# Kernel tuning notes

Measured on AMD Instinct MI355X. Metric: run time of the kernel, lower is better.

Reference implementation:

```python
import jax, jax.numpy as jnp
import numpy as np

B, D, H, E, C, TOPK = 16384, 2048, 2048, 6, 1024, 3

def setup_inputs() -> dict:
    key = jax.random.key(0)
    ks = jax.random.split(key, 8)
    s_d = 1.0 / np.sqrt(D)
    s_h = 1.0 / np.sqrt(H)
    return {
        "x": jax.random.normal(ks[0], (B, D), dtype=jnp.float32),
        "gate_W": jax.random.uniform(ks[1], (E, D), jnp.float32, -s_d, s_d),
        "gate_b": jax.random.uniform(ks[2], (E,), jnp.float32, -s_d, s_d),
        "W1": jax.random.uniform(ks[3], (E, H, D), jnp.float32, -s_d, s_d),
        "b1": jax.random.uniform(ks[4], (E, H), jnp.float32, -s_d, s_d),
        "W2": jax.random.uniform(ks[5], (E, C, H), jnp.float32, -s_h, s_h),
        "b2": jax.random.uniform(ks[6], (E, C), jnp.float32, -s_h, s_h),
    }

def reference(x, gate_W, gate_b, W1, b1, W2, b2):
    # gating: top-k sparse softmax
    gate_logits = x @ gate_W.T + gate_b                      # [B, E]
    topk_vals, topk_idx = jax.lax.top_k(gate_logits, TOPK)   # [B, K]
    neg_inf = jnp.finfo(gate_logits.dtype).min
    sparse = jnp.full_like(gate_logits, neg_inf)
    rows = jnp.arange(gate_logits.shape[0])[:, None]
    sparse = sparse.at[rows, topk_idx].set(topk_vals)
    gw = jax.nn.softmax(sparse, axis=-1)                     # [B, E]
    # dense experts: Linear -> GELU (exact, erf) -> Linear (dropout is eval no-op)
    h = jnp.einsum('bd,ehd->beh', x, W1) + b1[None]          # [B, E, H]
    h = jax.nn.gelu(h, approximate=False)
    expert_outs = jnp.einsum('beh,ech->bec', h, W2) + b2[None]  # [B, E, C]
    out = jnp.einsum('be,bec->bc', gw, expert_outs)          # masked combine
    return (out, gw)
```

## Files before the change

### kernel.cpp

```cpp
#include <hip/hip_runtime.h>
#include <hip/hip_bf16.h>
#include <math.h>

#define B_ 16384
#define D_ 2048
#define H_ 2048
#define E_ 6
#define C_ 1024

typedef __attribute__((ext_vector_type(8))) short short8;
typedef __attribute__((ext_vector_type(4))) float f32x4;

__device__ __forceinline__ unsigned short f2bf(float f) {
    __hip_bfloat16 h = __float2bfloat16(f);
    return *reinterpret_cast<unsigned short*>(&h);
}

__device__ __forceinline__ void async_copy16(const unsigned short* g, unsigned short* l) {
    __builtin_amdgcn_global_load_lds(
        (const __attribute__((address_space(1))) unsigned int*)(g),
        (__attribute__((address_space(3))) unsigned int*)(l), 16, 0, 0);
}

__global__ void gate_kernel(const float* __restrict__ x, const float* __restrict__ gW,
                            const float* __restrict__ gb, float* __restrict__ gw_out,
                            int* __restrict__ counts, int* __restrict__ rowlist,
                            float* __restrict__ wtslist) {
    int wave = threadIdx.x >> 6;
    int lane = threadIdx.x & 63;
    int row  = blockIdx.x * 4 + wave;
    const float* xr = x + (size_t)row * D_;
    double acc[E_] = {0, 0, 0, 0, 0, 0};
    for (int i = 0; i < D_ / 64; ++i) {
        int d = i * 64 + lane;
        double xv = (double)xr[d];
#pragma unroll
        for (int e = 0; e < E_; ++e) acc[e] += xv * (double)gW[e * D_ + d];
    }
#pragma unroll
    for (int off = 32; off > 0; off >>= 1) {
#pragma unroll
        for (int e = 0; e < E_; ++e) acc[e] += __shfl_down(acc[e], off);
    }
    if (lane == 0) {
        double lg[E_];
#pragma unroll
        for (int e = 0; e < E_; ++e) lg[e] = acc[e] + (double)gb[e];
        bool used[E_] = {false, false, false, false, false, false};
        int idx[3]; double val[3];
        for (int k = 0; k < 3; ++k) {
            int best = -1; double bv = -1e300;
            for (int e = 0; e < E_; ++e)
                if (!used[e] && lg[e] > bv) { bv = lg[e]; best = e; }
            used[best] = true; idx[k] = best; val[k] = bv;
        }
        double m = val[0];
        double w[3]; double s = 0.0;
        for (int k = 0; k < 3; ++k) { w[k] = exp(val[k] - m); s += w[k]; }
        float gwv[E_] = {0.f, 0.f, 0.f, 0.f, 0.f, 0.f};
        for (int k = 0; k < 3; ++k) gwv[idx[k]] = (float)(w[k] / s);
#pragma unroll
        for (int e = 0; e < E_; ++e) gw_out[(size_t)row * E_ + e] = gwv[e];
        for (int k = 0; k < 3; ++k) {
            int e = idx[k];
            int pos = atomicAdd(&counts[e], 1);
            rowlist[(size_t)e * B_ + pos] = row * 3 + k;
            wtslist[(size_t)e * B_ + pos] = (float)(w[k] / s);
        }
    }
}

__global__ void cast_f32_bf16(const float* __restrict__ in, unsigned short* __restrict__ out, int n4) {
    int i = blockIdx.x * blockDim.x + threadIdx.x;
    if (i < n4) {
        float4 v = ((const float4*)in)[i];
        ushort4 u;
        u.x = f2bf(v.x); u.y = f2bf(v.y); u.z = f2bf(v.z); u.w = f2bf(v.w);
        ((ushort4*)out)[i] = u;
    }
}

__global__ __launch_bounds__(256) void gemm1_kernel(
    const unsigned short* __restrict__ xb, const unsigned short* __restrict__ W1b,
    const float* __restrict__ b1, const int* __restrict__ counts,
    const int* __restrict__ rowlist, unsigned short* __restrict__ hbuf) {
    int e = blockIdx.z;
    int cnt = counts[e];
    int m0 = blockIdx.y * 128;
    if (m0 >= cnt) return;
    int n0 = blockIdx.x * 128;

    __shared__ __align__(16) unsigned short At[128 * 64];
    __shared__ __align__(16) unsigned short Bt[128 * 64];
    int tid = threadIdx.x;
    const int* rlist = rowlist + (size_t)e * B_;

    const unsigned short* aptr[4];
    const unsigned short* bptr[4];
#pragma unroll
    for (int it = 0; it < 4; ++it) {
        int seg = it * 256 + tid;
        int r = seg >> 3, c = seg & 7;
        int cs = c ^ (r & 7);
        int idx = m0 + r; if (idx >= cnt) idx = cnt - 1;
        aptr[it] = xb + (size_t)(rlist[idx] / 3) * D_ + cs * 8;
        bptr[it] = W1b + (size_t)e * H_ * D_ + (size_t)(n0 + r) * D_ + cs * 8;
    }
    int lane = tid & 63;
    int wv = tid >> 6;
    int wm = (wv & 1) * 64;
    int wn = (wv >> 1) * 64;
    int fm = lane & 15;
    int kg = lane >> 4;
    int fsw = fm & 7;
    f32x4 acc[4][4] = {};

    for (int k0 = 0; k0 < D_; k0 += 64) {
#pragma unroll
        for (int it = 0; it < 4; ++it) {
            async_copy16(aptr[it] + k0, At + (it * 256 + tid) * 8);
            async_copy16(bptr[it] + k0, Bt + (it * 256 + tid) * 8);
        }
        __syncthreads();
#pragma unroll
        for (int kk = 0; kk < 2; ++kk) {
            int g = kk * 4 + kg;
            int go = (g ^ fsw) * 8;
            short8 af[4], bfr[4];
#pragma unroll
            for (int mi = 0; mi < 4; ++mi)
                af[mi] = *(const short8*)(At + (wm + mi * 16 + fm) * 64 + go);
#pragma unroll
            for (int ni = 0; ni < 4; ++ni)
                bfr[ni] = *(const short8*)(Bt + (wn + ni * 16 + fm) * 64 + go);
#pragma unroll
            for (int mi = 0; mi < 4; ++mi)
#pragma unroll
                for (int ni = 0; ni < 4; ++ni)
                    acc[mi][ni] = __builtin_amdgcn_mfma_f32_16x16x32_bf16(af[mi], bfr[ni], acc[mi][ni], 0, 0, 0);
        }
        __syncthreads();
    }

    int rlim = cnt - m0;
#pragma unroll
    for (int mi = 0; mi < 4; ++mi) {
#pragma unroll
        for (int i = 0; i < 4; ++i) {
            int r = wm + mi * 16 + kg * 4 + i;
            if (r < rlim) {
                size_t base = (size_t)rlist[m0 + r] * H_ + n0;
#pragma unroll
                for (int ni = 0; ni < 4; ++ni) {
                    int col = wn + ni * 16 + fm;
                    float v = acc[mi][ni][i] + b1[e * H_ + n0 + col];
                    v = 0.5f * v * (1.0f + erff(v * 0.70710678118654752f));
                    hbuf[base + col] = f2bf(v);
                }
            }
        }
    }
}

__global__ __launch_bounds__(256) void gemm2_kernel(
    const unsigned short* __restrict__ hbuf, const unsigned short* __restrict__ W2b,
    const float* __restrict__ b2, const int* __restrict__ counts,
    const int* __restrict__ rowlist, const float* __restrict__ wtslist,
    float* __restrict__ out) {
    int e = blockIdx.z;
    int cnt = counts[e];
    int m0 = blockIdx.y * 128;
    if (m0 >= cnt) return;
    int n0 = blockIdx.x * 128;

    __shared__ __align__(16) unsigned short At[128 * 64];
    __shared__ __align__(16) unsigned short Bt[128 * 64];
    int tid = threadIdx.x;
    const int* rlist = rowlist + (size_t)e * B_;
    const float* wlist = wtslist + (size_t)e * B_;

    const unsigned short* aptr[4];
    const unsigned short* bptr[4];
#pragma unroll
    for (int it = 0; it < 4; ++it) {
        int seg = it * 256 + tid;
        int r = seg >> 3, c = seg & 7;
        int cs = c ^ (r & 7);
        int idx = m0 + r; if (idx >= cnt) idx = cnt - 1;
        aptr[it] = hbuf + (size_t)rlist[idx] * H_ + cs * 8;
        bptr[it] = W2b + (size_t)e * C_ * H_ + (size_t)(n0 + r) * H_ + cs * 8;
    }
    int lane = tid & 63;
    int wv = tid >> 6;
    int wm = (wv & 1) * 64;
    int wn = (wv >> 1) * 64;
    int fm = lane & 15;
    int kg = lane >> 4;
    int fsw = fm & 7;
    f32x4 acc[4][4] = {};

    for (int k0 = 0; k0 < H_; k0 += 64) {
#pragma unroll
        for (int it = 0; it < 4; ++it) {
            async_copy16(aptr[it] + k0, At + (it * 256 + tid) * 8);
            async_copy16(bptr[it] + k0, Bt + (it * 256 + tid) * 8);
        }
        __syncthreads();
#pragma unroll
        for (int kk = 0; kk < 2; ++kk) {
            int g = kk * 4 + kg;
            int go = (g ^ fsw) * 8;
            short8 af[4], bfr[4];
#pragma unroll
            for (int mi = 0; mi < 4; ++mi)
                af[mi] = *(const short8*)(At + (wm + mi * 16 + fm) * 64 + go);
#pragma unroll
            for (int ni = 0; ni < 4; ++ni)
                bfr[ni] = *(const short8*)(Bt + (wn + ni * 16 + fm) * 64 + go);
#pragma unroll
            for (int mi = 0; mi < 4; ++mi)
#pragma unroll
                for (int ni = 0; ni < 4; ++ni)
                    acc[mi][ni] = __builtin_amdgcn_mfma_f32_16x16x32_bf16(af[mi], bfr[ni], acc[mi][ni], 0, 0, 0);
        }
        __syncthreads();
    }

    int rlim = cnt - m0;
#pragma unroll
    for (int mi = 0; mi < 4; ++mi) {
#pragma unroll
        for (int i = 0; i < 4; ++i) {
            int r = wm + mi * 16 + kg * 4 + i;
            if (r < rlim) {
                float w = wlist[m0 + r];
                float* orow = out + (size_t)(rlist[m0 + r] / 3) * C_ + n0;
#pragma unroll
                for (int ni = 0; ni < 4; ++ni) {
                    int col = wn + ni * 16 + fm;
                    float v = (acc[mi][ni][i] + b2[e * C_ + n0 + col]) * w;
                    atomicAdd(&orow[col], v);
                }
            }
        }
    }
}

extern "C" void kernel_launch(void* const* d_in, const int* in_sizes, int n_in,
                              void* d_out, int out_size, void* d_ws, size_t ws_size,
                              hipStream_t stream) {
    const float* x  = (const float*)d_in[0];
    const float* gW = (const float*)d_in[1];
    const float* gb = (const float*)d_in[2];
    const float* W1 = (const float*)d_in[3];
    const float* b1 = (const float*)d_in[4];
    const float* W2 = (const float*)d_in[5];
    const float* b2 = (const float*)d_in[6];
    float* out    = (float*)d_out;
    float* gw_out = out + (size_t)B_ * C_;

    char* ws = (char*)d_ws;
    size_t off = 0;
    auto alloc = [&](size_t bytes) -> char* {
        char* p = ws + off;
        off = (off + bytes + 255) & ~(size_t)255;
        return p;
    };
    int*            counts  = (int*)alloc(E_ * 4);
    int*            rowlist = (int*)alloc((size_t)E_ * B_ * 4);
    float*          wtslist = (float*)alloc((size_t)E_ * B_ * 4);
    unsigned short* xb      = (unsigned short*)alloc((size_t)B_ * D_ * 2);
    unsigned short* W1b     = (unsigned short*)alloc((size_t)E_ * H_ * D_ * 2);
    unsigned short* W2b     = (unsigned short*)alloc((size_t)E_ * C_ * H_ * 2);
    unsigned short* hbuf    = (unsigned short*)alloc((size_t)3 * B_ * H_ * 2);
    (void)ws_size; (void)in_sizes; (void)n_in; (void)out_size;

    hipMemsetAsync(counts, 0, E_ * 4, stream);
    hipMemsetAsync(out, 0, (size_t)B_ * C_ * 4, stream);

    gate_kernel<<<B_ / 4, 256, 0, stream>>>(x, gW, gb, gw_out, counts, rowlist, wtslist);
    cast_f32_bf16<<<(B_ * D_ / 4) / 256, 256, 0, stream>>>(x, xb, B_ * D_ / 4);
    cast_f32_bf16<<<(E_ * H_ * D_ / 4) / 256, 256, 0, stream>>>(W1, W1b, E_ * H_ * D_ / 4);
    cast_f32_bf16<<<(E_ * C_ * H_ / 4) / 256, 256, 0, stream>>>(W2, W2b, E_ * C_ * H_ / 4);
    gemm1_kernel<<<dim3(H_ / 128, B_ / 128, E_), 256, 0, stream>>>(xb, W1b, b1, counts, rowlist, hbuf);
    gemm2_kernel<<<dim3(C_ / 128, B_ / 128, E_), 256, 0, stream>>>(hbuf, W2b, b2, counts, rowlist, wtslist, out);
}
```

Measured before the change: 2.089 ms.

## Triple-buffer GEMM pipeline with 256x128 tiles and replace atomics with slot combine

Rewrites both expert GEMM kernels to use 512-thread blocks over 256x128 tiles with a three-stage LDS ring buffer. Async global-to-LDS loads for step t+2 are interleaved with the MFMA work of step t, using explicit waitcnt, barriers and setprio. GEMM2 writes weighted per-slot results to a scratch buffer when workspace permits, and a separate combine kernel sums the three slots instead of using atomicAdd on the output. The aim is to hide memory latency, increase operand reuse and remove atomic contention. In exchange it uses more LDS (limiting occupancy), adds a large scratch write/read pass, and its correctness depends on hand-tuned wait counts.

```diff
diff --git a/kernel.cpp b/kernel.cpp
--- a/kernel.cpp
+++ b/kernel.cpp
@@ -80,79 +80,144 @@
     }
 }
 
-__global__ __launch_bounds__(256) void gemm1_kernel(
+
+#define GEMM_PROLOGUE_AND_LOOP(KDIM)                                                     \
+    int lane = tid & 63;                                                                 \
+    int wv   = tid >> 6;                                                                 \
+    int wrow = (wv >> 1) * 64;                                                           \
+    int wcol = (wv & 1) * 64;                                                            \
+    int fm   = lane & 15;                                                                \
+    int kg   = lane >> 4;                                                                \
+    int fsw  = fm & 7;                                                                   \
+    f32x4 acc[4][4] = {};                                                                \
+    unsigned short* A0 = As;                unsigned short* Bq0 = Bs;                    \
+    unsigned short* A1 = As + 256 * 64;     unsigned short* Bq1 = Bs + 128 * 64;         \
+    unsigned short* A2 = As + 2 * 256 * 64; unsigned short* Bq2 = Bs + 2 * 128 * 64;     \
+    _Pragma("unroll")                                                                    \
+    for (int it = 0; it < 4; ++it) async_copy16(aptr[it], A0 + (it * 512 + tid) * 8);    \
+    _Pragma("unroll")                                                                    \
+    for (int it = 0; it < 2; ++it) async_copy16(bptr[it], Bq0 + (it * 512 + tid) * 8);   \
+    _Pragma("unroll")                                                                    \
+    for (int it = 0; it < 4; ++it) async_copy16(aptr[it] + 64, A1 + (it * 512 + tid) * 8); \
+    _Pragma("unroll")                                                                    \
+    for (int it = 0; it < 2; ++it) async_copy16(bptr[it] + 64, Bq1 + (it * 512 + tid) * 8); \
+    asm volatile("s_waitcnt vmcnt(6)" ::: "memory");                                     \
+    __builtin_amdgcn_s_barrier();                                                        \
+    __builtin_amdgcn_sched_barrier(0);                                                   \
+    const int NT = (KDIM) / 64;                                                          \
+    for (int t = 0; t < NT; ++t) {                                                       \
+        const bool st  = (t + 2 < NT);                                                   \
+        const int  k0s = (t + 2) * 64;                                                   \
+        {                                              \
+            short8 aF[4], bF[4];                                                         \
+            int go = (kg ^ fsw) * 8;                                                     \
+            _Pragma("unroll")                                                            \
+            for (int mi = 0; mi < 4; ++mi)                                               \
+                aF[mi] = *(const short8*)(A0 + (wrow + mi * 16 + fm) * 64 + go);         \
+            _Pragma("unroll")                                                            \
+            for (int ni = 0; ni < 4; ++ni)                                               \
+                bF[ni] = *(const short8*)(Bq0 + (wcol + ni * 16 + fm) * 64 + go);        \
+            if (st) {                                                                    \
+                async_copy16(aptr[0] + k0s, A2 + (0 * 512 + tid) * 8);                   \
+                async_copy16(aptr[1] + k0s, A2 + (1 * 512 + tid) * 8);                   \
+                async_copy16(bptr[0] + k0s, Bq2 + (0 * 512 + tid) * 8);                  \
+            }                                                                            \
+            __builtin_amdgcn_s_barrier();                                                \
+            asm volatile("s_waitcnt lgkmcnt(0)" ::: "memory");                           \
+            __builtin_amdgcn_sched_barrier(0);                                           \
+            __builtin_amdgcn_s_setprio(1);                                               \
+            _Pragma("unroll")                                                            \
+            for (int mi = 0; mi < 4; ++mi)                                               \
+                _Pragma("unroll")                                                        \
+                for (int ni = 0; ni < 4; ++ni)                                           \
+                    acc[mi][ni] = __builtin_amdgcn_mfma_f32_16x16x32_bf16(               \
+                        aF[mi], bF[ni], acc[mi][ni], 0, 0, 0);                           \
+            __builtin_amdgcn_s_setprio(0);                                               \
+            __builtin_amdgcn_s_barrier();                                                \
+            __builtin_amdgcn_sched_barrier(0);                                           \
+        }                                                                                \
+        {                                              \
+            short8 aF[4], bF[4];                                                         \
+            int go = ((4 + kg) ^ fsw) * 8;                                               \
+            _Pragma("unroll")                                                            \
+            for (int mi = 0; mi < 4; ++mi)                                               \
+                aF[mi] = *(const short8*)(A0 + (wrow + mi * 16 + fm) * 64 + go);         \
+            _Pragma("unroll")                                                            \
+            for (int ni = 0; ni < 4; ++ni)                                               \
+                bF[ni] = *(const short8*)(Bq0 + (wcol + ni * 16 + fm) * 64 + go);        \
+            if (st) {                                                                    \
+                async_copy16(aptr[2] + k0s, A2 + (2 * 512 + tid) * 8);                   \
+                async_copy16(aptr[3] + k0s, A2 + (3 * 512 + tid) * 8);                   \
+                async_copy16(bptr[1] + k0s, Bq2 + (1 * 512 + tid) * 8);                  \
+            }                                                                            \
+            __builtin_amdgcn_s_barrier();                                                \
+            asm volatile("s_waitcnt lgkmcnt(0)" ::: "memory");                           \
+            __builtin_amdgcn_sched_barrier(0);                                           \
+            __builtin_amdgcn_s_setprio(1);                                               \
+            _Pragma("unroll")                                                            \
+            for (int mi = 0; mi < 4; ++mi)                                               \
+                _Pragma("unroll")                                                        \
+                for (int ni = 0; ni < 4; ++ni)                                           \
+                    acc[mi][ni] = __builtin_amdgcn_mfma_f32_16x16x32_bf16(               \
+                        aF[mi], bF[ni], acc[mi][ni], 0, 0, 0);                           \
+            __builtin_amdgcn_s_setprio(0);                                               \
+        }                                                                                \
+           \
+        if (st) asm volatile("s_waitcnt vmcnt(6)" ::: "memory");                         \
+        else    asm volatile("s_waitcnt vmcnt(0)" ::: "memory");                         \
+        __builtin_amdgcn_s_barrier();                                                    \
+        __builtin_amdgcn_sched_barrier(0);                                               \
+        unsigned short* tA = A0; A0 = A1; A1 = A2; A2 = tA;                              \
+        unsigned short* tB = Bq0; Bq0 = Bq1; Bq1 = Bq2; Bq2 = tB;                        \
+    }
+
+__global__ __launch_bounds__(512, 2) void gemm1_kernel(
     const unsigned short* __restrict__ xb, const unsigned short* __restrict__ W1b,
     const float* __restrict__ b1, const int* __restrict__ counts,
     const int* __restrict__ rowlist, unsigned short* __restrict__ hbuf) {
     int e = blockIdx.z;
     int cnt = counts[e];
-    int m0 = blockIdx.y * 128;
+    int m0 = blockIdx.y * 256;
     if (m0 >= cnt) return;
     int n0 = blockIdx.x * 128;
 
-    __shared__ __align__(16) unsigned short At[128 * 64];
-    __shared__ __align__(16) unsigned short Bt[128 * 64];
+    __shared__ __align__(16) unsigned short As[3 * 256 * 64];
+    __shared__ __align__(16) unsigned short Bs[3 * 128 * 64];
+
     int tid = threadIdx.x;
     const int* rlist = rowlist + (size_t)e * B_;
 
     const unsigned short* aptr[4];
-    const unsigned short* bptr[4];
+    const unsigned short* bptr[2];
 #pragma unroll
     for (int it = 0; it < 4; ++it) {
-        int seg = it * 256 + tid;
+        int seg = it * 512 + tid;
         int r = seg >> 3, c = seg & 7;
         int cs = c ^ (r & 7);
         int idx = m0 + r; if (idx >= cnt) idx = cnt - 1;
         aptr[it] = xb + (size_t)(rlist[idx] / 3) * D_ + cs * 8;
+    }
+#pragma unroll
+    for (int it = 0; it < 2; ++it) {
+        int seg = it * 512 + tid;
+        int r = seg >> 3, c = seg & 7;
+        int cs = c ^ (r & 7);
         bptr[it] = W1b + (size_t)e * H_ * D_ + (size_t)(n0 + r) * D_ + cs * 8;
     }
-    int lane = tid & 63;
-    int wv = tid >> 6;
-    int wm = (wv & 1) * 64;
-    int wn = (wv >> 1) * 64;
-    int fm = lane & 15;
-    int kg = lane >> 4;
-    int fsw = fm & 7;
-    f32x4 acc[4][4] = {};
-
-    for (int k0 = 0; k0 < D_; k0 += 64) {
-#pragma unroll
-        for (int it = 0; it < 4; ++it) {
-            async_copy16(aptr[it] + k0, At + (it * 256 + tid) * 8);
-            async_copy16(bptr[it] + k0, Bt + (it * 256 + tid) * 8);
-        }
-        __syncthreads();
-#pragma unroll
-        for (int kk = 0; kk < 2; ++kk) {
-            int g = kk * 4 + kg;
-            int go = (g ^ fsw) * 8;
-            short8 af[4], bfr[4];
-#pragma unroll
-            for (int mi = 0; mi < 4; ++mi)
-                af[mi] = *(const short8*)(At + (wm + mi * 16 + fm) * 64 + go);
-#pragma unroll
-            for (int ni = 0; ni < 4; ++ni)
-                bfr[ni] = *(const short8*)(Bt + (wn + ni * 16 + fm) * 64 + go);
-#pragma unroll
-            for (int mi = 0; mi < 4; ++mi)
-#pragma unroll
-                for (int ni = 0; ni < 4; ++ni)
-                    acc[mi][ni] = __builtin_amdgcn_mfma_f32_16x16x32_bf16(af[mi], bfr[ni], acc[mi][ni], 0, 0, 0);
-        }
-        __syncthreads();
-    }
+
+    GEMM_PROLOGUE_AND_LOOP(D_)
 
     int rlim = cnt - m0;
 #pragma unroll
     for (int mi = 0; mi < 4; ++mi) {
 #pragma unroll
         for (int i = 0; i < 4; ++i) {
-            int r = wm + mi * 16 + kg * 4 + i;
+            int r = wrow + mi * 16 + kg * 4 + i;
             if (r < rlim) {
                 size_t base = (size_t)rlist[m0 + r] * H_ + n0;
 #pragma unroll
                 for (int ni = 0; ni < 4; ++ni) {
-                    int col = wn + ni * 16 + fm;
+                    int col = wcol + ni * 16 + fm;
                     float v = acc[mi][ni][i] + b1[e * H_ + n0 + col];
                     v = 0.5f * v * (1.0f + erff(v * 0.70710678118654752f));
                     hbuf[base + col] = f2bf(v);
@@ -162,88 +227,84 @@
     }
 }
 
-__global__ __launch_bounds__(256) void gemm2_kernel(
+__global__ __launch_bounds__(512, 2) void gemm2_kernel(
     const unsigned short* __restrict__ hbuf, const unsigned short* __restrict__ W2b,
     const float* __restrict__ b2, const int* __restrict__ counts,
     const int* __restrict__ rowlist, const float* __restrict__ wtslist,
-    float* __restrict__ out) {
+    float* __restrict__ sbuf, float* __restrict__ out) {
     int e = blockIdx.z;
     int cnt = counts[e];
-    int m0 = blockIdx.y * 128;
+    int m0 = blockIdx.y * 256;
     if (m0 >= cnt) return;
     int n0 = blockIdx.x * 128;
 
-    __shared__ __align__(16) unsigned short At[128 * 64];
-    __shared__ __align__(16) unsigned short Bt[128 * 64];
+    __shared__ __align__(16) unsigned short As[3 * 256 * 64];
+    __shared__ __align__(16) unsigned short Bs[3 * 128 * 64];
+
     int tid = threadIdx.x;
     const int* rlist = rowlist + (size_t)e * B_;
     const float* wlist = wtslist + (size_t)e * B_;
 
     const unsigned short* aptr[4];
-    const unsigned short* bptr[4];
+    const unsigned short* bptr[2];
 #pragma unroll
     for (int it = 0; it < 4; ++it) {
-        int seg = it * 256 + tid;
+        int seg = it * 512 + tid;
         int r = seg >> 3, c = seg & 7;
         int cs = c ^ (r & 7);
         int idx = m0 + r; if (idx >= cnt) idx = cnt - 1;
         aptr[it] = hbuf + (size_t)rlist[idx] * H_ + cs * 8;
+    }
+#pragma unroll
+    for (int it = 0; it < 2; ++it) {
+        int seg = it * 512 + tid;
+        int r = seg >> 3, c = seg & 7;
+        int cs = c ^ (r & 7);
         bptr[it] = W2b + (size_t)e * C_ * H_ + (size_t)(n0 + r) * H_ + cs * 8;
     }
-    int lane = tid & 63;
-    int wv = tid >> 6;
-    int wm = (wv & 1) * 64;
-    int wn = (wv >> 1) * 64;
-    int fm = lane & 15;
-    int kg = lane >> 4;
-    int fsw = fm & 7;
-    f32x4 acc[4][4] = {};
-
-    for (int k0 = 0; k0 < H_; k0 += 64) {
-#pragma unroll
-        for (int it = 0; it < 4; ++it) {
-            async_copy16(aptr[it] + k0, At + (it * 256 + tid) * 8);
-            async_copy16(bptr[it] + k0, Bt + (it * 256 + tid) * 8);
-        }
-        __syncthreads();
-#pragma unroll
-        for (int kk = 0; kk < 2; ++kk) {
-            int g = kk * 4 + kg;
-            int go = (g ^ fsw) * 8;
-            short8 af[4], bfr[4];
-#pragma unroll
-            for (int mi = 0; mi < 4; ++mi)
-                af[mi] = *(const short8*)(At + (wm + mi * 16 + fm) * 64 + go);
-#pragma unroll
-            for (int ni = 0; ni < 4; ++ni)
-                bfr[ni] = *(const short8*)(Bt + (wn + ni * 16 + fm) * 64 + go);
-#pragma unroll
-            for (int mi = 0; mi < 4; ++mi)
-#pragma unroll
-                for (int ni = 0; ni < 4; ++ni)
-                    acc[mi][ni] = __builtin_amdgcn_mfma_f32_16x16x32_bf16(af[mi], bfr[ni], acc[mi][ni], 0, 0, 0);
-        }
-        __syncthreads();
-    }
+
+    GEMM_PROLOGUE_AND_LOOP(H_)
 
     int rlim = cnt - m0;
 #pragma unroll
     for (int mi = 0; mi < 4; ++mi) {
 #pragma unroll
         for (int i = 0; i < 4; ++i) {
-            int r = wm + mi * 16 + kg * 4 + i;
+            int r = wrow + mi * 16 + kg * 4 + i;
             if (r < rlim) {
-                float w = wlist[m0 + r];
-                float* orow = out + (size_t)(rlist[m0 + r] / 3) * C_ + n0;
-#pragma unroll
-                for (int ni = 0; ni < 4; ++ni) {
-                    int col = wn + ni * 16 + fm;
-                    float v = (acc[mi][ni][i] + b2[e * C_ + n0 + col]) * w;
-                    atomicAdd(&orow[col], v);
+                int slot = rlist[m0 + r];
+                float w  = wlist[m0 + r];
+                if (sbuf) {
+                    float* srow = sbuf + (size_t)slot * C_ + n0;
+#pragma unroll
+                    for (int ni = 0; ni < 4; ++ni) {
+                        int col = wcol + ni * 16 + fm;
+                        srow[col] = (acc[mi][ni][i] + b2[e * C_ + n0 + col]) * w;
+                    }
+                } else {
+                    float* orow = out + (size_t)(slot / 3) * C_ + n0;
+#pragma unroll
+                    for (int ni = 0; ni < 4; ++ni) {
+                        int col = wcol + ni * 16 + fm;
+                        atomicAdd(&orow[col], (acc[mi][ni][i] + b2[e * C_ + n0 + col]) * w);
+                    }
                 }
             }
         }
     }
+}
+
+__global__ void combine_kernel(const float* __restrict__ sbuf, float* __restrict__ out) {
+    int i   = blockIdx.x * 256 + threadIdx.x;
+    int row = i >> 8;
+    int c4  = i & 255;
+    const float4* s4 = (const float4*)sbuf;
+    size_t b = (size_t)row * 3 * 256 + c4;
+    float4 a = s4[b], d = s4[b + 256], g = s4[b + 512];
+    float4 r;
+    r.x = a.x + d.x + g.x; r.y = a.y + d.y + g.y;
+    r.z = a.z + d.z + g.z; r.w = a.w + d.w + g.w;
+    ((float4*)out)[i] = r;
 }
 
 extern "C" void kernel_launch(void* const* d_in, const int* in_sizes, int n_in,
@@ -273,15 +334,20 @@
     unsigned short* W1b     = (unsigned short*)alloc((size_t)E_ * H_ * D_ * 2);
     unsigned short* W2b     = (unsigned short*)alloc((size_t)E_ * C_ * H_ * 2);
     unsigned short* hbuf    = (unsigned short*)alloc((size_t)3 * B_ * H_ * 2);
-    (void)ws_size; (void)in_sizes; (void)n_in; (void)out_size;
+    float*          sbuf    = (float*)alloc((size_t)3 * B_ * C_ * 4);
+    bool use_sbuf = (ws_size == 0) || (off <= ws_size);
+    (void)in_sizes; (void)n_in; (void)out_size;
 
     hipMemsetAsync(counts, 0, E_ * 4, stream);
-    hipMemsetAsync(out, 0, (size_t)B_ * C_ * 4, stream);
+    if (!use_sbuf) hipMemsetAsync(out, 0, (size_t)B_ * C_ * 4, stream);
 
     gate_kernel<<<B_ / 4, 256, 0, stream>>>(x, gW, gb, gw_out, counts, rowlist, wtslist);
     cast_f32_bf16<<<(B_ * D_ / 4) / 256, 256, 0, stream>>>(x, xb, B_ * D_ / 4);
     cast_f32_bf16<<<(E_ * H_ * D_ / 4) / 256, 256, 0, stream>>>(W1, W1b, E_ * H_ * D_ / 4);
     cast_f32_bf16<<<(E_ * C_ * H_ / 4) / 256, 256, 0, stream>>>(W2, W2b, E_ * C_ * H_ / 4);
-    gemm1_kernel<<<dim3(H_ / 128, B_ / 128, E_), 256, 0, stream>>>(xb, W1b, b1, counts, rowlist, hbuf);
-    gemm2_kernel<<<dim3(C_ / 128, B_ / 128, E_), 256, 0, stream>>>(hbuf, W2b, b2, counts, rowlist, wtslist, out);
-}
+    gemm1_kernel<<<dim3(H_ / 128, B_ / 256, E_), 512, 0, stream>>>(xb, W1b, b1, counts, rowlist, hbuf);
+    gemm2_kernel<<<dim3(C_ / 128, B_ / 256, E_), 512, 0, stream>>>(hbuf, W2b, b2, counts, rowlist, wtslist,
+                                                                   use_sbuf ? sbuf : (float*)nullptr, out);
+    if (use_sbuf)
+        combine_kernel<<<(B_ * C_ / 4) / 256, 256, 0, stream>>>(sbuf, out);
+}
```

After: 2.088 ms. No clear change (-0.0%).
